# Kernel tuning notes

Measured on AMD Instinct MI355X. Metric: run time of the kernel, lower is better.

Reference implementation:

```python
import jax, jax.numpy as jnp
import numpy as np

MASK_RATIO = 0.02
N2V_W, WAV_W, TV_W = 1.0, 0.2, 0.01
THRESHOLD = 50.0
LEVELS = 3


def setup_inputs() -> dict:
    key = jax.random.key(0)
    k1, k2, k3 = jax.random.split(key, 3)
    shape = (64, 1, 512, 512)
    pred = jax.random.uniform(k1, shape, dtype=jnp.float32)
    noisy_input = jax.random.uniform(k2, shape, dtype=jnp.float32)
    # N2V random blind-spot mask (torch.rand_like(pred) < mask_ratio)
    mask = jax.random.uniform(k3, shape, dtype=jnp.float32) < MASK_RATIO
    return {"pred": pred, "noisy_input": noisy_input, "mask": mask}


def haar_dwt2(x):
    # x: [B, H, W] with H, W even. Single-level 2D Haar DWT (pywt 'haar').
    a = x[:, 0::2, 0::2]
    b = x[:, 0::2, 1::2]
    c = x[:, 1::2, 0::2]
    d = x[:, 1::2, 1::2]
    ll = (a + b + c + d) * 0.5
    ch = (a + b - c - d) * 0.5  # horizontal detail
    cv = (a - b + c - d) * 0.5  # vertical detail
    cd = (a - b - c + d) * 0.5  # diagonal detail
    return ll, ch, cv, cd


def _level_l1(c, thr):
    # L1 between coeff and its (detached) soft-thresholded version
    target = jax.lax.stop_gradient(jnp.sign(c) * jnp.maximum(jnp.abs(c) - thr, 0.0))
    return jnp.mean(jnp.abs(c - target))


def reference(pred, noisy_input, mask):
    p = jnp.clip(pred, 0.0, 1.0)

    # --- Noise2Void masked L1 ---
    m = mask.astype(p.dtype)
    n2v = jnp.sum(jnp.abs(p - noisy_input) * m) / jnp.maximum(jnp.sum(m), 1.0)

    # --- Wavelet sparsity (multi-level Haar, soft-threshold targets) ---
    x = p[:, 0]  # [B, H, W]
    details = []  # finest first
    for _ in range(LEVELS):
        x, ch, cv, cd = haar_dwt2(x)
        details.append((ch, cv, cd))
    wav = jnp.asarray(0.0, dtype=p.dtype)
    for level_idx in range(1, LEVELS + 1):  # level_idx=1 -> coarsest (wavedec2 order)
        ch, cv, cd = details[LEVELS - level_idx]
        thr = (THRESHOLD / (2.0 ** (level_idx - 1))) / 255.0
        lvl = (_level_l1(ch, thr) + _level_l1(cv, thr) + _level_l1(cd, thr)) / 3.0
        wav = wav + (1.0 / level_idx) * lvl

    # --- Total variation ---
    tv = jnp.mean(jnp.abs(p[:, :, 1:, :] - p[:, :, :-1, :])) + \
         jnp.mean(jnp.abs(p[:, :, :, 1:] - p[:, :, :, :-1]))

    return N2V_W * n2v + WAV_W * wav + TV_W * tv
```

## Files before the change

### kernel.cpp

```cpp
#include <hip/hip_runtime.h>

#define NIMG 64
#define H 512
#define W 512
#define HW (H * W)

typedef float f4 __attribute__((ext_vector_type(4)));
typedef int   i4 __attribute__((ext_vector_type(4)));

constexpr float THR_64  = 50.0f / 255.0f;
constexpr float THR_128 = 50.0f / 2.0f / 255.0f;
constexpr float THR_256 = 50.0f / 4.0f / 255.0f;

constexpr float SC_W1 = 0.2f  / 37748736.0f;
constexpr float SC_W2 = 0.2f  / 6291456.0f;
constexpr float SC_W3 = 0.2f  / 786432.0f;
constexpr float SC_TV = 0.01f / 16744448.0f;

__device__ __forceinline__ float wave_sum(float v) {
#pragma unroll
    for (int o = 32; o > 0; o >>= 1) v += __shfl_down(v, o, 64);
    return v;
}

__device__ __forceinline__ float clip01(float x) {
    return fminf(fmaxf(x, 0.0f), 1.0f);
}

__device__ __forceinline__ f4 clip4(f4 p) {
    p.x = clip01(p.x); p.y = clip01(p.y); p.z = clip01(p.z); p.w = clip01(p.w);
    return p;
}

__device__ __forceinline__ f4 ntl4(const float* p) {
    return __builtin_nontemporal_load(reinterpret_cast<const f4*>(p));
}
__device__ __forceinline__ i4 ntli(const int* p) {
    return __builtin_nontemporal_load(reinterpret_cast<const i4*>(p));
}

__global__ __launch_bounds__(128) void kA(const float* __restrict__ pred,
                                          const float* __restrict__ noisy,
                                          const int* __restrict__ mask,
                                          f4* __restrict__ pOut) {
    const int tid = threadIdx.x;
    const int lane = tid & 63;
    const int wv = tid >> 6;
    const int gw = (blockIdx.x << 1) + wv;
    const int n = gw >> 7;
    const int u = gw & 127;
    const int s = u >> 1;
    const int h = u & 1;
    const int r0 = s << 3;
    const int col0 = (h << 8) + (lane << 2);
    const size_t img = (size_t)n * HW;
    const size_t base = img + (size_t)r0 * W + col0;

    i4 m[8];
#pragma unroll
    for (int r = 0; r < 8; ++r)
        m[r] = ntli(mask + base + (size_t)r * W);

    f4 p[8];
#pragma unroll
    for (int r = 0; r < 8; ++r)
        p[r] = ntl4(pred + base + (size_t)r * W);

    f4 hl = {0.f, 0.f, 0.f, 0.f};
    if (r0 > 0)
        hl = ntl4(pred + base - W);

    float smv = 0.f;
    if (h == 0 && lane < 8)
        smv = pred[img + (size_t)(r0 + lane) * W + 256];

    f4 nz[8];
#pragma unroll
    for (int r = 0; r < 8; ++r) {
        nz[r] = (f4){0.f, 0.f, 0.f, 0.f};
        if ((m[r].x | m[r].y | m[r].z | m[r].w) != 0)
            nz[r] = ntl4(noisy + base + (size_t)r * W);
    }

#pragma unroll
    for (int r = 0; r < 8; ++r) p[r] = clip4(p[r]);
    hl = clip4(hl);
    smv = clip01(smv);

    float tv = 0.0f;
#pragma unroll
    for (int r = 0; r < 8; ++r) {
        const f4 q = p[r];
        tv += fabsf(q.y - q.x) + fabsf(q.z - q.y) + fabsf(q.w - q.z);
        float nb = __shfl_down(q.x, 1, 64);
        float seam_r = __shfl(smv, r, 64);
        if (lane == 63) nb = seam_r;
        if (lane < 63 || h == 0) tv += fabsf(nb - q.w);
    }
#pragma unroll
    for (int r = 0; r < 7; ++r) {
        tv += fabsf(p[r + 1].x - p[r].x) + fabsf(p[r + 1].y - p[r].y)
            + fabsf(p[r + 1].z - p[r].z) + fabsf(p[r + 1].w - p[r].w);
    }
    if (r0 > 0) {
        tv += fabsf(p[0].x - hl.x) + fabsf(p[0].y - hl.y)
            + fabsf(p[0].z - hl.z) + fabsf(p[0].w - hl.w);
    }

    float ll1[4][2];
    float wav1 = 0.0f;
#pragma unroll
    for (int rp = 0; rp < 4; ++rp) {
        const f4 t = p[2 * rp];
        const f4 bo = p[2 * rp + 1];
        float a, b, c, d, ch, cv, cd;
        a = t.x; b = t.y; c = bo.x; d = bo.y;
        ll1[rp][0] = (a + b + c + d) * 0.5f;
        ch = (a + b - c - d) * 0.5f; cv = (a - b + c - d) * 0.5f; cd = (a - b - c + d) * 0.5f;
        wav1 += fminf(fabsf(ch), THR_256) + fminf(fabsf(cv), THR_256) + fminf(fabsf(cd), THR_256);
        a = t.z; b = t.w; c = bo.z; d = bo.w;
        ll1[rp][1] = (a + b + c + d) * 0.5f;
        ch = (a + b - c - d) * 0.5f; cv = (a - b + c - d) * 0.5f; cd = (a - b - c + d) * 0.5f;
        wav1 += fminf(fabsf(ch), THR_256) + fminf(fabsf(cv), THR_256) + fminf(fabsf(cd), THR_256);
    }

    float ll2[2];
    float wav2 = 0.0f;
#pragma unroll
    for (int lp = 0; lp < 2; ++lp) {
        const float a = ll1[2 * lp][0], b = ll1[2 * lp][1];
        const float c = ll1[2 * lp + 1][0], d = ll1[2 * lp + 1][1];
        ll2[lp] = (a + b + c + d) * 0.5f;
        const float ch = (a + b - c - d) * 0.5f;
        const float cv = (a - b + c - d) * 0.5f;
        const float cd = (a - b - c + d) * 0.5f;
        wav2 += fminf(fabsf(ch), THR_128) + fminf(fabsf(cv), THR_128) + fminf(fabsf(cd), THR_128);
    }

    float w3 = 0.0f;
    {
        const float b3 = __shfl_xor(ll2[0], 1, 64);
        const float d3 = __shfl_xor(ll2[1], 1, 64);
        if ((lane & 1) == 0) {
            const float a = ll2[0], b = b3, c = ll2[1], d = d3;
            const float ch = (a + b - c - d) * 0.5f;
            const float cv = (a - b + c - d) * 0.5f;
            const float cd = (a - b - c + d) * 0.5f;
            w3 = fminf(fabsf(ch), THR_64) + fminf(fabsf(cv), THR_64)
               + fminf(fabsf(cd), THR_64);
        }
    }

    float n2v = 0.0f, msum = 0.0f;
#pragma unroll
    for (int r = 0; r < 8; ++r) {
        float mm;
        mm = m[r].x ? 1.f : 0.f; n2v += fabsf(p[r].x - nz[r].x) * mm; msum += mm;
        mm = m[r].y ? 1.f : 0.f; n2v += fabsf(p[r].y - nz[r].y) * mm; msum += mm;
        mm = m[r].z ? 1.f : 0.f; n2v += fabsf(p[r].z - nz[r].z) * mm; msum += mm;
        mm = m[r].w ? 1.f : 0.f; n2v += fabsf(p[r].w - nz[r].w) * mm; msum += mm;
    }

    const float comb = wav1 * SC_W1 + wav2 * SC_W2 + w3 * SC_W3 + tv * SC_TV;

    float v0 = wave_sum(n2v);
    float v1 = wave_sum(msum);
    float v2 = wave_sum(comb);
    if (lane == 0) {
        f4 o = {v0, v1, v2, 0.f};
        pOut[gw] = o;
    }
}

__global__ __launch_bounds__(256) void kD(const f4* __restrict__ pA,
                                          float* __restrict__ out) {
    __shared__ float red[4][3];
    const int tid = threadIdx.x;
    const int lane = tid & 63, wv = tid >> 6;

    float s0 = 0, s1 = 0, s2 = 0;
#pragma unroll
    for (int j = 0; j < 32; ++j) {
        f4 v = pA[tid + (j << 8)];
        s0 += v.x; s1 += v.y; s2 += v.z;
    }
    s0 = wave_sum(s0); s1 = wave_sum(s1); s2 = wave_sum(s2);
    if (lane == 0) {
        red[wv][0] = s0; red[wv][1] = s1; red[wv][2] = s2;
    }
    __syncthreads();
    if (tid == 0) {
        float a0 = red[0][0] + red[1][0] + red[2][0] + red[3][0];
        float a1 = red[0][1] + red[1][1] + red[2][1] + red[3][1];
        float a2 = red[0][2] + red[1][2] + red[2][2] + red[3][2];
        out[0] = a0 / fmaxf(a1, 1.0f) + a2;
    }
}

extern "C" void kernel_launch(void* const* d_in, const int* in_sizes, int n_in,
                              void* d_out, int out_size, void* d_ws, size_t ws_size,
                              hipStream_t stream) {
    (void)in_sizes; (void)n_in; (void)out_size; (void)ws_size;
    const float* pred  = (const float*)d_in[0];
    const float* noisy = (const float*)d_in[1];
    const int*   mask  = (const int*)d_in[2];

    f4* pA = (f4*)d_ws;

    kA<<<4096, 128, 0, stream>>>(pred, noisy, mask, pA);
    kD<<<1, 256, 0, stream>>>(pA, (float*)d_out);
}
```

Baseline: 192.5 us.

## Stream rows in a rolled loop to cut registers and raise occupancy

Each wave now processes its 8-row strip as four iterations of two rows each, instead of loading all 8 rows of mask, pred and noisy up front. The level-2 Haar and TV row differences are carried across iterations, and blocks grow to 256 threads with a launch-bounds occupancy hint. Nontemporal loads are replaced by normal loads. The aim is to lower register pressure so more waves fit per CU to hide memory latency. The cost is less memory-level parallelism per wave, because the rolled loop serialises its loads.

```diff
diff --git a/kernel.cpp b/kernel.cpp
--- a/kernel.cpp
+++ b/kernel.cpp
@@ -32,21 +32,14 @@
     return p;
 }
 
-__device__ __forceinline__ f4 ntl4(const float* p) {
-    return __builtin_nontemporal_load(reinterpret_cast<const f4*>(p));
-}
-__device__ __forceinline__ i4 ntli(const int* p) {
-    return __builtin_nontemporal_load(reinterpret_cast<const i4*>(p));
-}
-
-__global__ __launch_bounds__(128) void kA(const float* __restrict__ pred,
-                                          const float* __restrict__ noisy,
-                                          const int* __restrict__ mask,
-                                          f4* __restrict__ pOut) {
+__global__ __launch_bounds__(256, 4) void kA(const float* __restrict__ pred,
+                                             const float* __restrict__ noisy,
+                                             const int* __restrict__ mask,
+                                             f4* __restrict__ pOut) {
     const int tid = threadIdx.x;
     const int lane = tid & 63;
     const int wv = tid >> 6;
-    const int gw = (blockIdx.x << 1) + wv;
+    const int gw = (blockIdx.x << 2) + wv;
     const int n = gw >> 7;
     const int u = gw & 127;
     const int s = u >> 1;
@@ -56,109 +49,111 @@
     const size_t img = (size_t)n * HW;
     const size_t base = img + (size_t)r0 * W + col0;
 
-    i4 m[8];
-#pragma unroll
-    for (int r = 0; r < 8; ++r)
-        m[r] = ntli(mask + base + (size_t)r * W);
-
-    f4 p[8];
-#pragma unroll
-    for (int r = 0; r < 8; ++r)
-        p[r] = ntl4(pred + base + (size_t)r * W);
-
-    f4 hl = {0.f, 0.f, 0.f, 0.f};
-    if (r0 > 0)
-        hl = ntl4(pred + base - W);
+    const float* pb = pred + base;
+    const float* nb = noisy + base;
+    const int*   mb = mask + base;
 
     float smv = 0.f;
     if (h == 0 && lane < 8)
         smv = pred[img + (size_t)(r0 + lane) * W + 256];
-
-    f4 nz[8];
-#pragma unroll
-    for (int r = 0; r < 8; ++r) {
-        nz[r] = (f4){0.f, 0.f, 0.f, 0.f};
-        if ((m[r].x | m[r].y | m[r].z | m[r].w) != 0)
-            nz[r] = ntl4(noisy + base + (size_t)r * W);
-    }
-
-#pragma unroll
-    for (int r = 0; r < 8; ++r) p[r] = clip4(p[r]);
-    hl = clip4(hl);
     smv = clip01(smv);
 
-    float tv = 0.0f;
-#pragma unroll
-    for (int r = 0; r < 8; ++r) {
-        const f4 q = p[r];
-        tv += fabsf(q.y - q.x) + fabsf(q.z - q.y) + fabsf(q.w - q.z);
-        float nb = __shfl_down(q.x, 1, 64);
-        float seam_r = __shfl(smv, r, 64);
-        if (lane == 63) nb = seam_r;
-        if (lane < 63 || h == 0) tv += fabsf(nb - q.w);
-    }
-#pragma unroll
-    for (int r = 0; r < 7; ++r) {
-        tv += fabsf(p[r + 1].x - p[r].x) + fabsf(p[r + 1].y - p[r].y)
-            + fabsf(p[r + 1].z - p[r].z) + fabsf(p[r + 1].w - p[r].w);
-    }
-    if (r0 > 0) {
-        tv += fabsf(p[0].x - hl.x) + fabsf(p[0].y - hl.y)
-            + fabsf(p[0].z - hl.z) + fabsf(p[0].w - hl.w);
-    }
-
-    float ll1[4][2];
-    float wav1 = 0.0f;
-#pragma unroll
-    for (int rp = 0; rp < 4; ++rp) {
-        const f4 t = p[2 * rp];
-        const f4 bo = p[2 * rp + 1];
+    f4 prev = {0.f, 0.f, 0.f, 0.f};
+    if (r0 > 0)
+        prev = clip4(*reinterpret_cast<const f4*>(pb - W));
+
+    float n2v = 0.f, msum = 0.f, tv = 0.f, wav1 = 0.f, wav2 = 0.f;
+    float ll1pa = 0.f, ll1pb = 0.f;
+    float ll2A = 0.f, ll2B = 0.f;
+
+#pragma unroll 1
+    for (int it = 0; it < 4; ++it) {
+        const i4 m0 = *reinterpret_cast<const i4*>(mb);
+        const i4 m1 = *reinterpret_cast<const i4*>(mb + W);
+        f4 p0 = *reinterpret_cast<const f4*>(pb);
+        f4 p1 = *reinterpret_cast<const f4*>(pb + W);
+        f4 nz0 = {0.f, 0.f, 0.f, 0.f}, nz1 = {0.f, 0.f, 0.f, 0.f};
+        if ((m0.x | m0.y | m0.z | m0.w) != 0)
+            nz0 = *reinterpret_cast<const f4*>(nb);
+        if ((m1.x | m1.y | m1.z | m1.w) != 0)
+            nz1 = *reinterpret_cast<const f4*>(nb + W);
+        pb += 2 * W; nb += 2 * W; mb += 2 * W;
+
+        p0 = clip4(p0);
+        p1 = clip4(p1);
+
+        {
+            float mm;
+            mm = m0.x ? 1.f : 0.f; n2v += fabsf(p0.x - nz0.x) * mm; msum += mm;
+            mm = m0.y ? 1.f : 0.f; n2v += fabsf(p0.y - nz0.y) * mm; msum += mm;
+            mm = m0.z ? 1.f : 0.f; n2v += fabsf(p0.z - nz0.z) * mm; msum += mm;
+            mm = m0.w ? 1.f : 0.f; n2v += fabsf(p0.w - nz0.w) * mm; msum += mm;
+            mm = m1.x ? 1.f : 0.f; n2v += fabsf(p1.x - nz1.x) * mm; msum += mm;
+            mm = m1.y ? 1.f : 0.f; n2v += fabsf(p1.y - nz1.y) * mm; msum += mm;
+            mm = m1.z ? 1.f : 0.f; n2v += fabsf(p1.z - nz1.z) * mm; msum += mm;
+            mm = m1.w ? 1.f : 0.f; n2v += fabsf(p1.w - nz1.w) * mm; msum += mm;
+        }
+
+        {
+            const f4 q = p0;
+            tv += fabsf(q.y - q.x) + fabsf(q.z - q.y) + fabsf(q.w - q.z);
+            float nbx = __shfl_down(q.x, 1, 64);
+            const float se = __shfl(smv, 2 * it, 64);
+            if (lane == 63) nbx = se;
+            if (lane < 63 || h == 0) tv += fabsf(nbx - q.w);
+        }
+        {
+            const f4 q = p1;
+            tv += fabsf(q.y - q.x) + fabsf(q.z - q.y) + fabsf(q.w - q.z);
+            float nbx = __shfl_down(q.x, 1, 64);
+            const float se = __shfl(smv, 2 * it + 1, 64);
+            if (lane == 63) nbx = se;
+            if (lane < 63 || h == 0) tv += fabsf(nbx - q.w);
+        }
+
+        if (it + r0 > 0) {
+            tv += fabsf(p0.x - prev.x) + fabsf(p0.y - prev.y)
+                + fabsf(p0.z - prev.z) + fabsf(p0.w - prev.w);
+        }
+        tv += fabsf(p1.x - p0.x) + fabsf(p1.y - p0.y)
+            + fabsf(p1.z - p0.z) + fabsf(p1.w - p0.w);
+        prev = p1;
+
         float a, b, c, d, ch, cv, cd;
-        a = t.x; b = t.y; c = bo.x; d = bo.y;
-        ll1[rp][0] = (a + b + c + d) * 0.5f;
+        a = p0.x; b = p0.y; c = p1.x; d = p1.y;
+        const float lla = (a + b + c + d) * 0.5f;
         ch = (a + b - c - d) * 0.5f; cv = (a - b + c - d) * 0.5f; cd = (a - b - c + d) * 0.5f;
         wav1 += fminf(fabsf(ch), THR_256) + fminf(fabsf(cv), THR_256) + fminf(fabsf(cd), THR_256);
-        a = t.z; b = t.w; c = bo.z; d = bo.w;
-        ll1[rp][1] = (a + b + c + d) * 0.5f;
+        a = p0.z; b = p0.w; c = p1.z; d = p1.w;
+        const float llb = (a + b + c + d) * 0.5f;
         ch = (a + b - c - d) * 0.5f; cv = (a - b + c - d) * 0.5f; cd = (a - b - c + d) * 0.5f;
         wav1 += fminf(fabsf(ch), THR_256) + fminf(fabsf(cv), THR_256) + fminf(fabsf(cd), THR_256);
-    }
-
-    float ll2[2];
-    float wav2 = 0.0f;
-#pragma unroll
-    for (int lp = 0; lp < 2; ++lp) {
-        const float a = ll1[2 * lp][0], b = ll1[2 * lp][1];
-        const float c = ll1[2 * lp + 1][0], d = ll1[2 * lp + 1][1];
-        ll2[lp] = (a + b + c + d) * 0.5f;
-        const float ch = (a + b - c - d) * 0.5f;
-        const float cv = (a - b + c - d) * 0.5f;
-        const float cd = (a - b - c + d) * 0.5f;
-        wav2 += fminf(fabsf(ch), THR_128) + fminf(fabsf(cv), THR_128) + fminf(fabsf(cd), THR_128);
+
+        if (it & 1) {
+            a = ll1pa; b = ll1pb; c = lla; d = llb;
+            const float ll2v = (a + b + c + d) * 0.5f;
+            ch = (a + b - c - d) * 0.5f;
+            cv = (a - b + c - d) * 0.5f;
+            cd = (a - b - c + d) * 0.5f;
+            wav2 += fminf(fabsf(ch), THR_128) + fminf(fabsf(cv), THR_128) + fminf(fabsf(cd), THR_128);
+            if (it == 1) ll2A = ll2v; else ll2B = ll2v;
+        } else {
+            ll1pa = lla; ll1pb = llb;
+        }
     }
 
     float w3 = 0.0f;
     {
-        const float b3 = __shfl_xor(ll2[0], 1, 64);
-        const float d3 = __shfl_xor(ll2[1], 1, 64);
+        const float b3 = __shfl_xor(ll2A, 1, 64);
+        const float d3 = __shfl_xor(ll2B, 1, 64);
         if ((lane & 1) == 0) {
-            const float a = ll2[0], b = b3, c = ll2[1], d = d3;
+            const float a = ll2A, b = b3, c = ll2B, d = d3;
             const float ch = (a + b - c - d) * 0.5f;
             const float cv = (a - b + c - d) * 0.5f;
             const float cd = (a - b - c + d) * 0.5f;
             w3 = fminf(fabsf(ch), THR_64) + fminf(fabsf(cv), THR_64)
                + fminf(fabsf(cd), THR_64);
         }
-    }
-
-    float n2v = 0.0f, msum = 0.0f;
-#pragma unroll
-    for (int r = 0; r < 8; ++r) {
-        float mm;
-        mm = m[r].x ? 1.f : 0.f; n2v += fabsf(p[r].x - nz[r].x) * mm; msum += mm;
-        mm = m[r].y ? 1.f : 0.f; n2v += fabsf(p[r].y - nz[r].y) * mm; msum += mm;
-        mm = m[r].z ? 1.f : 0.f; n2v += fabsf(p[r].z - nz[r].z) * mm; msum += mm;
-        mm = m[r].w ? 1.f : 0.f; n2v += fabsf(p[r].w - nz[r].w) * mm; msum += mm;
     }
 
     const float comb = wav1 * SC_W1 + wav2 * SC_W2 + w3 * SC_W3 + tv * SC_TV;
@@ -207,6 +202,6 @@
 
     f4* pA = (f4*)d_ws;
 
-    kA<<<4096, 128, 0, stream>>>(pred, noisy, mask, pA);
+    kA<<<2048, 256, 0, stream>>>(pred, noisy, mask, pA);
     kD<<<1, 256, 0, stream>>>(pA, (float*)d_out);
 }
```

Result: no change. 194.2 us (+0.9%).
